# Optimization experiments

Measured on AMD Instinct MI355X. Metric: run time of the kernel, lower is better.

## Reference

```python
import jax, jax.numpy as jnp
import numpy as np

N_TOKENS = 4096
HIDDEN = 1024
FFN = 2048
N_EXPERTS = 8
TOP_K = 2


def setup_inputs() -> dict:
    key = jax.random.key(0)
    k1, k2, k3, k4 = jax.random.split(key, 4)
    x = jax.random.normal(k1, (N_TOKENS, HIDDEN), dtype=jnp.float32)
    router_weight = jax.random.normal(k2, (HIDDEN, N_EXPERTS), dtype=jnp.float32)
    # matches torch.randn(...) * 0.02 init scale
    w1 = jax.random.normal(k3, (HIDDEN, FFN * N_EXPERTS), dtype=jnp.float32) * 0.02
    w2 = jax.random.normal(k4, (FFN * N_EXPERTS, HIDDEN), dtype=jnp.float32) * 0.02
    return {"x": x, "router_weight": router_weight, "w1": w1, "w2": w2, "top_k": TOP_K}


def reference(x, router_weight, w1, w2, top_k):
    # x: [N, H]; router_weight: [H, E]; w1: [H, E*F]; w2: [E*F, H]
    N, H = x.shape
    E = router_weight.shape[1]
    F = w1.shape[1] // E

    # --- routing (router in fp32, softmax over experts, top-k probs) ---
    logits = x.astype(jnp.float32) @ router_weight            # [N, E]
    probs = jax.nn.softmax(logits, axis=-1)                   # [N, E]
    topk_probs, topk_idx = jax.lax.top_k(probs, top_k)        # [N, k]

    # --- expert FFN: per-expert gelu(x @ w1_e) @ w2_e ---
    # Dense formulation: compute every expert for every token, then gather the
    # top-k outputs per token. Same math as grouped-GEMM dispatch/combine.
    h = jax.nn.gelu(x @ w1, approximate=False)                # [N, E*F]
    h = h.reshape(N, E, F)
    w2e = w2.reshape(E, F, H)
    y = jnp.einsum('nef,efh->neh', h, w2e)                    # [N, E, H]

    # --- combine: weight selected expert outputs by router probs, sum top-k ---
    sel = jnp.take_along_axis(y, topk_idx[:, :, None], axis=1)   # [N, k, H]
    out = (sel * topk_probs[:, :, None].astype(sel.dtype)).sum(axis=1)  # [N, H]
    return out
```

## Files before the change

### kernel.cpp

```cpp
#include <hip/hip_runtime.h>
#include <hip/hip_bf16.h>
#include <math.h>

#define N_TOK 4096
#define HID   1024
#define FFN   2048
#define NEXP  8
#define WROW  (NEXP*FFN)
#define NSLOT (N_TOK*2)
#define NCHUNK (NSLOT/64)

typedef __attribute__((ext_vector_type(4))) float f32x4;
typedef __attribute__((ext_vector_type(8))) short short8;

__device__ inline unsigned short f2bf(float f) {
  union { float f; unsigned u; } v; v.f = f;
  unsigned r = v.u + 0x7fffu + ((v.u >> 16) & 1u);
  return (unsigned short)(r >> 16);
}
__device__ __forceinline__ float bf2f(unsigned short u) {
  union { unsigned u; float f; } v; v.u = ((unsigned)u) << 16; return v.f;
}

__device__ __forceinline__ void gload16(const void* g, void* l) {
  __builtin_amdgcn_global_load_lds((const __attribute__((address_space(1))) void*)g,
                                   (__attribute__((address_space(3))) void*)l, 16, 0, 0);
}

__global__ __launch_bounds__(256) void router_kernel(
    const float* __restrict__ x, const float* __restrict__ rw,
    int* __restrict__ eidx, float* __restrict__ probs,
    unsigned short* __restrict__ xb) {
  __shared__ float rwT[NEXP][HID];
  const int t = threadIdx.x;
  #pragma unroll
  for (int it = 0; it < 8; ++it) {
    const int flat = t * 4 + it * 1024;
    const f32x4 v = *(const f32x4*)&rw[flat];
    #pragma unroll
    for (int j = 0; j < 4; ++j) rwT[(flat + j) & 7][(flat + j) >> 3] = v[j];
  }
  __syncthreads();

  const int w = t >> 6, l = t & 63;
  const int n = blockIdx.x * 4 + w;
  const float* xr = x + (size_t)n * HID;
  float acc[NEXP];
  #pragma unroll
  for (int e = 0; e < NEXP; ++e) acc[e] = 0.f;

  #pragma unroll
  for (int j = 0; j < 4; ++j) {
    const int i = l * 4 + j * 256;
    const f32x4 xv = *(const f32x4*)&xr[i];
    if (xb) {
      ushort4 o;
      o.x = f2bf(xv[0]); o.y = f2bf(xv[1]); o.z = f2bf(xv[2]); o.w = f2bf(xv[3]);
      *(ushort4*)&xb[(size_t)n * HID + i] = o;
    }
    #pragma unroll
    for (int e = 0; e < NEXP; ++e) {
      const f32x4 wv = *(const f32x4*)&rwT[e][i];
      acc[e] += xv[0] * wv[0] + xv[1] * wv[1] + xv[2] * wv[2] + xv[3] * wv[3];
    }
  }
  #pragma unroll
  for (int e = 0; e < NEXP; ++e) {
    float s = acc[e];
    #pragma unroll
    for (int off = 32; off; off >>= 1) s += __shfl_xor(s, off);
    acc[e] = s;
  }
  if (l == 0) {
    float m = acc[0];
    #pragma unroll
    for (int e = 1; e < NEXP; ++e) m = fmaxf(m, acc[e]);
    float p[NEXP]; float den = 0.f;
    #pragma unroll
    for (int e = 0; e < NEXP; ++e) { p[e] = expf(acc[e] - m); den += p[e]; }
    const float inv = 1.f / den;
    int e1 = 0; float b1 = -1.f;
    #pragma unroll
    for (int e = 0; e < NEXP; ++e) if (p[e] > b1) { b1 = p[e]; e1 = e; }
    int e2 = 0; float b2 = -1.f;
    #pragma unroll
    for (int e = 0; e < NEXP; ++e) if (e != e1 && p[e] > b2) { b2 = p[e]; e2 = e; }
    eidx[n * 2 + 0] = e1; eidx[n * 2 + 1] = e2;
    probs[n * 2 + 0] = b1 * inv; probs[n * 2 + 1] = b2 * inv;
  }
}

__global__ __launch_bounds__(256) void dispatch_kernel(
    const int* __restrict__ eidx, const float* __restrict__ probs,
    int* __restrict__ counts, int* __restrict__ offs,
    int* __restrict__ rowtok, float* __restrict__ rowprob,
    int* __restrict__ tokslot) {
  __shared__ int chunkbase[NCHUNK][NEXP];
  __shared__ int tot[NEXP], off_s[NEXP];
  const int t = threadIdx.x;
  const int w = t >> 6, l = t & 63;

  for (int c = w; c < NCHUNK; c += 4) {
    const int e = eidx[c * 64 + l];
    #pragma unroll
    for (int xp = 0; xp < NEXP; ++xp) {
      const unsigned long long m = __ballot(e == xp);
      if (l == xp) chunkbase[c][xp] = __popcll(m);
    }
  }
  __syncthreads();

  if (t < NEXP) {
    int a = 0;
    for (int c = 0; c < NCHUNK; ++c) {
      const int v = chunkbase[c][t];
      chunkbase[c][t] = a;
      a += v;
    }
    tot[t] = a;
  }
  __syncthreads();
  if (t == 0) {
    int a = 0;
    for (int e = 0; e < NEXP; ++e) { off_s[e] = a; offs[e] = a; counts[e] = tot[e]; a += tot[e]; }
  }
  __syncthreads();

  for (int c = w; c < NCHUNK; c += 4) {
    const int s = c * 64 + l;
    const int e = eidx[s];
    unsigned long long mask_e = 0;
    #pragma unroll
    for (int xp = 0; xp < NEXP; ++xp) {
      const unsigned long long m = __ballot(e == xp);
      if (e == xp) mask_e = m;
    }
    const unsigned long long below = mask_e & ((1ull << l) - 1ull);
    const int pos = off_s[e] + chunkbase[c][e] + __popcll(below);
    rowtok[pos]  = s >> 1;
    rowprob[pos] = probs[s];
    tokslot[s]   = pos;
  }
}

__global__ __launch_bounds__(256) void tconv_kernel(
    const float* __restrict__ in, unsigned short* __restrict__ out,
    int R, int C, int RB) {
  __shared__ float tile[64][65];
  const int r0 = blockIdx.y * 64, c0 = blockIdx.x * 64;
  const int t = threadIdx.x;
  const int tr = t >> 4;
  const int tc4 = (t & 15) * 4;
  #pragma unroll
  for (int i = 0; i < 4; ++i) {
    const int r = tr + i * 16;
    const f32x4 v = *(const f32x4*)&in[(size_t)(r0 + r) * C + c0 + tc4];
    tile[r][tc4 + 0] = v[0]; tile[r][tc4 + 1] = v[1];
    tile[r][tc4 + 2] = v[2]; tile[r][tc4 + 3] = v[3];
  }
  __syncthreads();
  const int eb  = r0 / RB;
  const int rm0 = r0 % RB;
  #pragma unroll
  for (int i = 0; i < 4; ++i) {
    const int c = tr + i * 16;
    ushort4 o;
    o.x = f2bf(tile[tc4 + 0][c]); o.y = f2bf(tile[tc4 + 1][c]);
    o.z = f2bf(tile[tc4 + 2][c]); o.w = f2bf(tile[tc4 + 3][c]);
    const size_t oidx = (size_t)eb * C * RB + (size_t)(c0 + c) * RB + rm0 + tc4;
    *(ushort4*)&out[oidx] = o;
  }
}

__global__ __launch_bounds__(256) void gemm1_fast(
    const unsigned short* __restrict__ xb, const unsigned short* __restrict__ w1t,
    const int* __restrict__ rowtok, const int* __restrict__ counts,
    const int* __restrict__ offs, unsigned short* __restrict__ h1) {
  const int e   = blockIdx.z;
  const int cnt = counts[e];
  const int m0  = blockIdx.y * 128;
  if (m0 >= cnt) return;
  const int n0  = blockIdx.x * 128;
  const int seg = offs[e];

  __shared__ alignas(16) unsigned short Al[128 * 32];
  __shared__ alignas(16) unsigned short Bl[128 * 32];

  const int t  = threadIdx.x;
  const int l  = t & 63;
  const int w  = t >> 6;
  const int wr = w >> 1, wc = w & 1;
  const int lr = l & 15, hi = l >> 4;

  const int rowS = t >> 2;
  const int kc   = (t & 3) * 8;
  const int ra0 = m0 + rowS      < cnt ? m0 + rowS      : cnt - 1;
  const int ra1 = m0 + rowS + 64 < cnt ? m0 + rowS + 64 : cnt - 1;
  const unsigned short* aptr0 = xb + (size_t)rowtok[seg + ra0] * HID + kc;
  const unsigned short* aptr1 = xb + (size_t)rowtok[seg + ra1] * HID + kc;
  const unsigned short* bptr0 = w1t + ((size_t)e * FFN + n0 + rowS)      * HID + kc;
  const unsigned short* bptr1 = w1t + ((size_t)e * FFN + n0 + rowS + 64) * HID + kc;
  unsigned short* const ldsA0 = Al + (t & 192) * 8;
  unsigned short* const ldsB0 = Bl + (t & 192) * 8;

  f32x4 acc[4][4];
  #pragma unroll
  for (int i = 0; i < 4; ++i)
    #pragma unroll
    for (int j = 0; j < 4; ++j) acc[i][j] = (f32x4){0.f, 0.f, 0.f, 0.f};

  for (int k0 = 0; k0 < HID; k0 += 32) {
    gload16(aptr0 + k0, ldsA0);
    gload16(aptr1 + k0, ldsA0 + 2048);
    gload16(bptr0 + k0, ldsB0);
    gload16(bptr1 + k0, ldsB0 + 2048);
    __syncthreads();
    short8 af[4], bfr[4];
    #pragma unroll
    for (int mi = 0; mi < 4; ++mi) af[mi]  = *(const short8*)&Al[(wr * 64 + mi * 16 + lr) * 32 + hi * 8];
    #pragma unroll
    for (int ni = 0; ni < 4; ++ni) bfr[ni] = *(const short8*)&Bl[(wc * 64 + ni * 16 + lr) * 32 + hi * 8];
    #pragma unroll
    for (int mi = 0; mi < 4; ++mi)
      #pragma unroll
      for (int ni = 0; ni < 4; ++ni)
        acc[mi][ni] = __builtin_amdgcn_mfma_f32_16x16x32_bf16(af[mi], bfr[ni], acc[mi][ni], 0, 0, 0);
    __syncthreads();
  }

  #pragma unroll
  for (int mi = 0; mi < 4; ++mi) {
    #pragma unroll
    for (int r = 0; r < 4; ++r) {
      const int grow = m0 + wr * 64 + mi * 16 + hi * 4 + r;
      if (grow < cnt) {
        const size_t rowoff = (size_t)(seg + grow) * FFN + n0 + wc * 64 + lr;
        #pragma unroll
        for (int ni = 0; ni < 4; ++ni) {
          const float v = acc[mi][ni][r];
          const float g = 0.5f * v * (1.0f + erff(v * 0.70710678118654752f));
          h1[rowoff + ni * 16] = f2bf(g);
        }
      }
    }
  }
}

template<int KS>
__global__ __launch_bounds__(256) void gemm2_fast(
    const unsigned short* __restrict__ h1, const unsigned short* __restrict__ w2t,
    const int* __restrict__ counts, const int* __restrict__ offs,
    unsigned short* __restrict__ y) {
  const int e   = blockIdx.z & 7;
  const int kz  = blockIdx.z >> 3;
  const int cnt = counts[e];
  const int m0  = blockIdx.y * 128;
  if (m0 >= cnt) return;
  const int n0  = blockIdx.x * 128;
  const int seg = offs[e];
  constexpr int KLEN = FFN / KS;
  const int kbase = kz * KLEN;

  __shared__ alignas(16) unsigned short Al[128 * 32];
  __shared__ alignas(16) unsigned short Bl[128 * 32];

  const int t  = threadIdx.x;
  const int l  = t & 63;
  const int w  = t >> 6;
  const int wr = w >> 1, wc = w & 1;
  const int lr = l & 15, hi = l >> 4;

  const int rowS = t >> 2;
  const int kc   = (t & 3) * 8;
  const int ra0 = m0 + rowS      < cnt ? m0 + rowS      : cnt - 1;
  const int ra1 = m0 + rowS + 64 < cnt ? m0 + rowS + 64 : cnt - 1;
  const unsigned short* aptr0 = h1 + (size_t)(seg + ra0) * FFN + kbase + kc;
  const unsigned short* aptr1 = h1 + (size_t)(seg + ra1) * FFN + kbase + kc;
  const unsigned short* bptr0 = w2t + ((size_t)e * HID + n0 + rowS)      * FFN + kbase + kc;
  const unsigned short* bptr1 = w2t + ((size_t)e * HID + n0 + rowS + 64) * FFN + kbase + kc;
  unsigned short* const ldsA0 = Al + (t & 192) * 8;
  unsigned short* const ldsB0 = Bl + (t & 192) * 8;

  f32x4 acc[4][4];
  #pragma unroll
  for (int i = 0; i < 4; ++i)
    #pragma unroll
    for (int j = 0; j < 4; ++j) acc[i][j] = (f32x4){0.f, 0.f, 0.f, 0.f};

  for (int k0 = 0; k0 < KLEN; k0 += 32) {
    gload16(aptr0 + k0, ldsA0);
    gload16(aptr1 + k0, ldsA0 + 2048);
    gload16(bptr0 + k0, ldsB0);
    gload16(bptr1 + k0, ldsB0 + 2048);
    __syncthreads();
    short8 af[4], bfr[4];
    #pragma unroll
    for (int mi = 0; mi < 4; ++mi) af[mi]  = *(const short8*)&Al[(wr * 64 + mi * 16 + lr) * 32 + hi * 8];
    #pragma unroll
    for (int ni = 0; ni < 4; ++ni) bfr[ni] = *(const short8*)&Bl[(wc * 64 + ni * 16 + lr) * 32 + hi * 8];
    #pragma unroll
    for (int mi = 0; mi < 4; ++mi)
      #pragma unroll
      for (int ni = 0; ni < 4; ++ni)
        acc[mi][ni] = __builtin_amdgcn_mfma_f32_16x16x32_bf16(af[mi], bfr[ni], acc[mi][ni], 0, 0, 0);
    __syncthreads();
  }

  #pragma unroll
  for (int mi = 0; mi < 4; ++mi) {
    #pragma unroll
    for (int r = 0; r < 4; ++r) {
      const int grow = m0 + wr * 64 + mi * 16 + hi * 4 + r;
      if (grow < cnt) {
        const int slot = seg + grow;
        unsigned short* yrow = y + ((size_t)kz * NSLOT + slot) * HID + n0 + wc * 64 + lr;
        #pragma unroll
        for (int ni = 0; ni < 4; ++ni)
          yrow[ni * 16] = f2bf(acc[mi][ni][r]);
      }
    }
  }
}

template<int KS>
__global__ __launch_bounds__(256) void combine_kernel(
    const unsigned short* __restrict__ y, const int* __restrict__ tokslot,
    const float* __restrict__ probs, float* __restrict__ out) {
  const int n = blockIdx.x;
  const int c = threadIdx.x * 4;
  const int s1 = tokslot[n * 2 + 0], s2 = tokslot[n * 2 + 1];
  const float p1 = probs[n * 2 + 0], p2 = probs[n * 2 + 1];
  float r0 = 0.f, r1 = 0.f, r2 = 0.f, r3 = 0.f;
  #pragma unroll
  for (int kz = 0; kz < KS; ++kz) {
    const ushort4 a = *(const ushort4*)&y[((size_t)kz * NSLOT + s1) * HID + c];
    const ushort4 b = *(const ushort4*)&y[((size_t)kz * NSLOT + s2) * HID + c];
    r0 += p1 * bf2f(a.x) + p2 * bf2f(b.x);
    r1 += p1 * bf2f(a.y) + p2 * bf2f(b.y);
    r2 += p1 * bf2f(a.z) + p2 * bf2f(b.z);
    r3 += p1 * bf2f(a.w) + p2 * bf2f(b.w);
  }
  *(f32x4*)&out[(size_t)n * HID + c] = (f32x4){r0, r1, r2, r3};
}

__global__ __launch_bounds__(256) void gemm2_fast_atomic(
    const unsigned short* __restrict__ h1, const unsigned short* __restrict__ w2t,
    const int* __restrict__ rowtok, const float* __restrict__ rowprob,
    const int* __restrict__ counts, const int* __restrict__ offs,
    float* __restrict__ out) {
  const int e   = blockIdx.z;
  const int cnt = counts[e];
  const int m0  = blockIdx.y * 128;
  if (m0 >= cnt) return;
  const int n0  = blockIdx.x * 128;
  const int seg = offs[e];

  __shared__ alignas(16) unsigned short Al[128 * 32];
  __shared__ alignas(16) unsigned short Bl[128 * 32];

  const int t  = threadIdx.x;
  const int l  = t & 63;
  const int w  = t >> 6;
  const int wr = w >> 1, wc = w & 1;
  const int lr = l & 15, hi = l >> 4;

  const int rowS = t >> 2;
  const int kc   = (t & 3) * 8;
  const int ra0 = m0 + rowS      < cnt ? m0 + rowS      : cnt - 1;
  const int ra1 = m0 + rowS + 64 < cnt ? m0 + rowS + 64 : cnt - 1;
  const unsigned short* aptr0 = h1 + (size_t)(seg + ra0) * FFN + kc;
  const unsigned short* aptr1 = h1 + (size_t)(seg + ra1) * FFN + kc;
  const unsigned short* bptr0 = w2t + ((size_t)e * HID + n0 + rowS)      * FFN + kc;
  const unsigned short* bptr1 = w2t + ((size_t)e * HID + n0 + rowS + 64) * FFN + kc;
  unsigned short* const ldsA0 = Al + (t & 192) * 8;
  unsigned short* const ldsB0 = Bl + (t & 192) * 8;

  f32x4 acc[4][4];
  #pragma unroll
  for (int i = 0; i < 4; ++i)
    #pragma unroll
    for (int j = 0; j < 4; ++j) acc[i][j] = (f32x4){0.f, 0.f, 0.f, 0.f};

  for (int k0 = 0; k0 < FFN; k0 += 32) {
    gload16(aptr0 + k0, ldsA0);
    gload16(aptr1 + k0, ldsA0 + 2048);
    gload16(bptr0 + k0, ldsB0);
    gload16(bptr1 + k0, ldsB0 + 2048);
    __syncthreads();
    short8 af[4], bfr[4];
    #pragma unroll
    for (int mi = 0; mi < 4; ++mi) af[mi]  = *(const short8*)&Al[(wr * 64 + mi * 16 + lr) * 32 + hi * 8];
    #pragma unroll
    for (int ni = 0; ni < 4; ++ni) bfr[ni] = *(const short8*)&Bl[(wc * 64 + ni * 16 + lr) * 32 + hi * 8];
    #pragma unroll
    for (int mi = 0; mi < 4; ++mi)
      #pragma unroll
      for (int ni = 0; ni < 4; ++ni)
        acc[mi][ni] = __builtin_amdgcn_mfma_f32_16x16x32_bf16(af[mi], bfr[ni], acc[mi][ni], 0, 0, 0);
    __syncthreads();
  }

  #pragma unroll
  for (int mi = 0; mi < 4; ++mi) {
    #pragma unroll
    for (int r = 0; r < 4; ++r) {
      const int grow = m0 + wr * 64 + mi * 16 + hi * 4 + r;
      if (grow < cnt) {
        const int slot = seg + grow;
        const int tok  = rowtok[slot];
        const float p  = rowprob[slot];
        #pragma unroll
        for (int ni = 0; ni < 4; ++ni)
          atomicAdd(&out[(size_t)tok * HID + n0 + wc * 64 + ni * 16 + lr], p * acc[mi][ni][r]);
      }
    }
  }
}

__global__ __launch_bounds__(256) void gemm1_old(
    const float* __restrict__ x, const float* __restrict__ w1,
    const int* __restrict__ rowtok, const int* __restrict__ counts,
    const int* __restrict__ offs, unsigned short* __restrict__ h1) {
  const int e   = blockIdx.z;
  const int cnt = counts[e];
  const int m0  = blockIdx.y * 64;
  if (m0 >= cnt) return;
  const int n0  = blockIdx.x * 64;
  const int seg = offs[e];
  __shared__ unsigned short Al[64 * 40];
  __shared__ unsigned short Bl[64 * 40];
  const int t  = threadIdx.x;
  const int l  = t & 63;
  const int wv = t >> 6;
  const int wr = wv >> 1, wc = wv & 1;
  const int am  = t >> 2;
  const int akb = (t & 3) * 8;
  const int amg = m0 + am;
  const bool aval = (amg < cnt);
  const float* aptr = aval ? (x + (size_t)rowtok[seg + amg] * HID + akb) : x;
  const int bn  = t & 63;
  const int bkg = (t >> 6) * 8;
  const float* bptr = w1 + (size_t)e * FFN + n0 + bn;
  f32x4 acc[2][2];
  #pragma unroll
  for (int i = 0; i < 2; ++i)
    #pragma unroll
    for (int j = 0; j < 2; ++j) acc[i][j] = (f32x4){0.f, 0.f, 0.f, 0.f};
  const int kreg = (l >> 4) * 8;
  const int lr   = l & 15;
  for (int k0 = 0; k0 < HID; k0 += 32) {
    short8 av = (short8){0,0,0,0,0,0,0,0};
    if (aval) {
      const f32x4 v0 = *(const f32x4*)(aptr + k0);
      const f32x4 v1 = *(const f32x4*)(aptr + k0 + 4);
      #pragma unroll
      for (int j = 0; j < 4; ++j) { av[j] = (short)f2bf(v0[j]); av[4 + j] = (short)f2bf(v1[j]); }
    }
    *(short8*)&Al[am * 40 + akb] = av;
    short8 bv;
    #pragma unroll
    for (int j = 0; j < 8; ++j) bv[j] = (short)f2bf(bptr[(size_t)(k0 + bkg + j) * WROW]);
    *(short8*)&Bl[bn * 40 + bkg] = bv;
    __syncthreads();
    short8 af[2], bfr[2];
    #pragma unroll
    for (int mi = 0; mi < 2; ++mi) af[mi]  = *(const short8*)&Al[(wr * 32 + mi * 16 + lr) * 40 + kreg];
    #pragma unroll
    for (int ni = 0; ni < 2; ++ni) bfr[ni] = *(const short8*)&Bl[(wc * 32 + ni * 16 + lr) * 40 + kreg];
    #pragma unroll
    for (int mi = 0; mi < 2; ++mi)
      #pragma unroll
      for (int ni = 0; ni < 2; ++ni)
        acc[mi][ni] = __builtin_amdgcn_mfma_f32_16x16x32_bf16(af[mi], bfr[ni], acc[mi][ni], 0, 0, 0);
    __syncthreads();
  }
  const int kq = l >> 4;
  #pragma unroll
  for (int mi = 0; mi < 2; ++mi) {
    #pragma unroll
    for (int r = 0; r < 4; ++r) {
      const int grow = m0 + wr * 32 + mi * 16 + kq * 4 + r;
      if (grow < cnt) {
        #pragma unroll
        for (int ni = 0; ni < 2; ++ni) {
          const float v = acc[mi][ni][r];
          const float g = 0.5f * v * (1.0f + erff(v * 0.70710678118654752f));
          h1[(size_t)(seg + grow) * FFN + n0 + wc * 32 + ni * 16 + lr] = f2bf(g);
        }
      }
    }
  }
}

__global__ __launch_bounds__(256) void gemm2_old(
    const unsigned short* __restrict__ h1, const float* __restrict__ w2,
    const int* __restrict__ rowtok, const float* __restrict__ rowprob,
    const int* __restrict__ counts, const int* __restrict__ offs,
    float* __restrict__ out) {
  const int e   = blockIdx.z;
  const int cnt = counts[e];
  const int m0  = blockIdx.y * 64;
  if (m0 >= cnt) return;
  const int n0  = blockIdx.x * 64;
  const int seg = offs[e];
  __shared__ unsigned short Al[64 * 40];
  __shared__ unsigned short Bl[64 * 40];
  const int t  = threadIdx.x;
  const int l  = t & 63;
  const int wv = t >> 6;
  const int wr = wv >> 1, wc = wv & 1;
  const int am  = t >> 2;
  const int akb = (t & 3) * 8;
  const int amg = m0 + am;
  const bool aval = (amg < cnt);
  const unsigned short* aptr = aval ? (h1 + (size_t)(seg + amg) * FFN + akb) : h1;
  const int bn  = t & 63;
  const int bkg = (t >> 6) * 8;
  const float* bptr = w2 + (size_t)e * FFN * HID + n0 + bn;
  f32x4 acc[2][2];
  #pragma unroll
  for (int i = 0; i < 2; ++i)
    #pragma unroll
    for (int j = 0; j < 2; ++j) acc[i][j] = (f32x4){0.f, 0.f, 0.f, 0.f};
  const int kreg = (l >> 4) * 8;
  const int lr   = l & 15;
  for (int k0 = 0; k0 < FFN; k0 += 32) {
    short8 av = (short8){0,0,0,0,0,0,0,0};
    if (aval) av = *(const short8*)(aptr + k0);
    *(short8*)&Al[am * 40 + akb] = av;
    short8 bv;
    #pragma unroll
    for (int j = 0; j < 8; ++j) bv[j] = (short)f2bf(bptr[(size_t)(k0 + bkg + j) * HID]);
    *(short8*)&Bl[bn * 40 + bkg] = bv;
    __syncthreads();
    short8 af[2], bfr[2];
    #pragma unroll
    for (int mi = 0; mi < 2; ++mi) af[mi]  = *(const short8*)&Al[(wr * 32 + mi * 16 + lr) * 40 + kreg];
    #pragma unroll
    for (int ni = 0; ni < 2; ++ni) bfr[ni] = *(const short8*)&Bl[(wc * 32 + ni * 16 + lr) * 40 + kreg];
    #pragma unroll
    for (int mi = 0; mi < 2; ++mi)
      #pragma unroll
      for (int ni = 0; ni < 2; ++ni)
        acc[mi][ni] = __builtin_amdgcn_mfma_f32_16x16x32_bf16(af[mi], bfr[ni], acc[mi][ni], 0, 0, 0);
    __syncthreads();
  }
  const int kq = l >> 4;
  #pragma unroll
  for (int mi = 0; mi < 2; ++mi) {
    #pragma unroll
    for (int r = 0; r < 4; ++r) {
      const int grow = m0 + wr * 32 + mi * 16 + kq * 4 + r;
      if (grow < cnt) {
        const int slot = seg + grow;
        const int tok  = rowtok[slot];
        const float p  = rowprob[slot];
        #pragma unroll
        for (int ni = 0; ni < 2; ++ni)
          atomicAdd(&out[(size_t)tok * HID + n0 + wc * 32 + ni * 16 + lr], p * acc[mi][ni][r]);
      }
    }
  }
}

extern "C" void kernel_launch(void* const* d_in, const int* in_sizes, int n_in,
                              void* d_out, int out_size, void* d_ws, size_t ws_size,
                              hipStream_t stream) {
  const float* x  = (const float*)d_in[0];
  const float* rw = (const float*)d_in[1];
  const float* w1 = (const float*)d_in[2];
  const float* w2 = (const float*)d_in[3];
  float* out = (float*)d_out;

  int*   counts  = (int*)d_ws;
  int*   offs    = counts + 8;
  int*   tokslot = counts + 16;
  int*   eidx    = tokslot + NSLOT;
  float* probs   = (float*)(eidx + NSLOT);
  int*   rowtok  = (int*)(probs + NSLOT);
  float* rowprob = (float*)(rowtok + NSLOT);
  unsigned short* h1 = (unsigned short*)(rowprob + NSLOT);
  unsigned short* xb = h1 + (size_t)NSLOT * FFN;
  unsigned short* wt = xb + (size_t)N_TOK * HID;
  unsigned short* y  = wt + (size_t)WROW * HID;

  const size_t need_base = (size_t)((char*)y - (char*)d_ws);
  const size_t need_y1   = need_base + (size_t)NSLOT * HID * 2;
  const size_t need_y2   = need_base + (size_t)2 * NSLOT * HID * 2;
  const bool fast = (ws_size >= need_base);

  router_kernel<<<N_TOK / 4, 256, 0, stream>>>(x, rw, eidx, probs, fast ? xb : nullptr);
  dispatch_kernel<<<1, 256, 0, stream>>>(eidx, probs, counts, offs, rowtok, rowprob, tokslot);

  if (fast) {
    tconv_kernel<<<dim3(WROW / 64, HID / 64), 256, 0, stream>>>(w1, wt, HID, WROW, HID);
    gemm1_fast<<<dim3(FFN / 128, NSLOT / 128, NEXP), 256, 0, stream>>>(xb, wt, rowtok, counts, offs, h1);
    tconv_kernel<<<dim3(HID / 64, WROW / 64), 256, 0, stream>>>(w2, wt, WROW, HID, FFN);
    if (ws_size >= need_y2) {
      gemm2_fast<2><<<dim3(HID / 128, NSLOT / 128, NEXP * 2), 256, 0, stream>>>(h1, wt, counts, offs, y);
      combine_kernel<2><<<N_TOK, 256, 0, stream>>>(y, tokslot, probs, out);
    } else if (ws_size >= need_y1) {
      gemm2_fast<1><<<dim3(HID / 128, NSLOT / 128, NEXP), 256, 0, stream>>>(h1, wt, counts, offs, y);
      combine_kernel<1><<<N_TOK, 256, 0, stream>>>(y, tokslot, probs, out);
    } else {
      hipMemsetAsync(d_out, 0, (size_t)out_size * sizeof(float), stream);
      gemm2_fast_atomic<<<dim3(HID / 128, NSLOT / 128, NEXP), 256, 0, stream>>>(h1, wt, rowtok, rowprob, counts, offs, out);
    }
  } else {
    hipMemsetAsync(d_out, 0, (size_t)out_size * sizeof(float), stream);
    gemm1_old<<<dim3(FFN / 64, NSLOT / 64, NEXP), 256, 0, stream>>>(x, w1, rowtok, counts, offs, h1);
    gemm2_old<<<dim3(HID / 64, NSLOT / 64, NEXP), 256, 0, stream>>>(h1, w2, rowtok, rowprob, counts, offs, out);
  }
}
```

Measured before the change: 223.1 us.

## Double-buffer LDS tiles in expert GEMMs and use fast tanh-form GELU

```diff
diff --git a/kernel.cpp b/kernel.cpp
--- a/kernel.cpp
+++ b/kernel.cpp
@@ -20,6 +20,11 @@
 }
 __device__ __forceinline__ float bf2f(unsigned short u) {
   union { unsigned u; float f; } v; v.u = ((unsigned)u) << 16; return v.f;
+}
+
+__device__ __forceinline__ float gelu_f(float v) {
+  const float u = 1.5957691216057308f * v + 0.07135481627f * (v * v * v);
+  return v / (1.f + __expf(-u));
 }
 
 __device__ __forceinline__ void gload16(const void* g, void* l) {
@@ -183,8 +188,8 @@
   const int n0  = blockIdx.x * 128;
   const int seg = offs[e];
 
-  __shared__ alignas(16) unsigned short Al[128 * 32];
-  __shared__ alignas(16) unsigned short Bl[128 * 32];
+  __shared__ alignas(16) unsigned short Al[2][128 * 32];
+  __shared__ alignas(16) unsigned short Bl[2][128 * 32];
 
   const int t  = threadIdx.x;
   const int l  = t & 63;
@@ -200,8 +205,7 @@
   const unsigned short* aptr1 = xb + (size_t)rowtok[seg + ra1] * HID + kc;
   const unsigned short* bptr0 = w1t + ((size_t)e * FFN + n0 + rowS)      * HID + kc;
   const unsigned short* bptr1 = w1t + ((size_t)e * FFN + n0 + rowS + 64) * HID + kc;
-  unsigned short* const ldsA0 = Al + (t & 192) * 8;
-  unsigned short* const ldsB0 = Bl + (t & 192) * 8;
+  const int ldst = (t & 192) * 8;
 
   f32x4 acc[4][4];
   #pragma unroll
@@ -209,22 +213,33 @@
     #pragma unroll
     for (int j = 0; j < 4; ++j) acc[i][j] = (f32x4){0.f, 0.f, 0.f, 0.f};
 
-  for (int k0 = 0; k0 < HID; k0 += 32) {
-    gload16(aptr0 + k0, ldsA0);
-    gload16(aptr1 + k0, ldsA0 + 2048);
-    gload16(bptr0 + k0, ldsB0);
-    gload16(bptr1 + k0, ldsB0 + 2048);
-    __syncthreads();
+  auto STAGE = [&](int b, int k0) {
+    gload16(aptr0 + k0, &Al[b][ldst]);
+    gload16(aptr1 + k0, &Al[b][ldst + 2048]);
+    gload16(bptr0 + k0, &Bl[b][ldst]);
+    gload16(bptr1 + k0, &Bl[b][ldst + 2048]);
+  };
+  auto COMPUTE = [&](int b) {
     short8 af[4], bfr[4];
     #pragma unroll
-    for (int mi = 0; mi < 4; ++mi) af[mi]  = *(const short8*)&Al[(wr * 64 + mi * 16 + lr) * 32 + hi * 8];
-    #pragma unroll
-    for (int ni = 0; ni < 4; ++ni) bfr[ni] = *(const short8*)&Bl[(wc * 64 + ni * 16 + lr) * 32 + hi * 8];
+    for (int mi = 0; mi < 4; ++mi) af[mi]  = *(const short8*)&Al[b][(wr * 64 + mi * 16 + lr) * 32 + hi * 8];
+    #pragma unroll
+    for (int ni = 0; ni < 4; ++ni) bfr[ni] = *(const short8*)&Bl[b][(wc * 64 + ni * 16 + lr) * 32 + hi * 8];
     #pragma unroll
     for (int mi = 0; mi < 4; ++mi)
       #pragma unroll
       for (int ni = 0; ni < 4; ++ni)
         acc[mi][ni] = __builtin_amdgcn_mfma_f32_16x16x32_bf16(af[mi], bfr[ni], acc[mi][ni], 0, 0, 0);
+  };
+
+  STAGE(0, 0);
+  __syncthreads();
+  for (int k0 = 0; k0 < HID; k0 += 64) {
+    STAGE(1, k0 + 32);
+    COMPUTE(0);
+    __syncthreads();
+    if (k0 + 64 < HID) STAGE(0, k0 + 64);
+    COMPUTE(1);
     __syncthreads();
   }
 
@@ -236,11 +251,8 @@
       if (grow < cnt) {
         const size_t rowoff = (size_t)(seg + grow) * FFN + n0 + wc * 64 + lr;
         #pragma unroll
-        for (int ni = 0; ni < 4; ++ni) {
-          const float v = acc[mi][ni][r];
-          const float g = 0.5f * v * (1.0f + erff(v * 0.70710678118654752f));
-          h1[rowoff + ni * 16] = f2bf(g);
-        }
+        for (int ni = 0; ni < 4; ++ni)
+          h1[rowoff + ni * 16] = f2bf(gelu_f(acc[mi][ni][r]));
       }
     }
   }
@@ -261,8 +273,8 @@
   constexpr int KLEN = FFN / KS;
   const int kbase = kz * KLEN;
 
-  __shared__ alignas(16) unsigned short Al[128 * 32];
-  __shared__ alignas(16) unsigned short Bl[128 * 32];
+  __shared__ alignas(16) unsigned short Al[2][128 * 32];
+  __shared__ alignas(16) unsigned short Bl[2][128 * 32];
 
   const int t  = threadIdx.x;
   const int l  = t & 63;
@@ -278,8 +290,7 @@
   const unsigned short* aptr1 = h1 + (size_t)(seg + ra1) * FFN + kbase + kc;
   const unsigned short* bptr0 = w2t + ((size_t)e * HID + n0 + rowS)      * FFN + kbase + kc;
   const unsigned short* bptr1 = w2t + ((size_t)e * HID + n0 + rowS + 64) * FFN + kbase + kc;
-  unsigned short* const ldsA0 = Al + (t & 192) * 8;
-  unsigned short* const ldsB0 = Bl + (t & 192) * 8;
+  const int ldst = (t & 192) * 8;
 
   f32x4 acc[4][4];
   #pragma unroll
@@ -287,22 +298,33 @@
     #pragma unroll
     for (int j = 0; j < 4; ++j) acc[i][j] = (f32x4){0.f, 0.f, 0.f, 0.f};
 
-  for (int k0 = 0; k0 < KLEN; k0 += 32) {
-    gload16(aptr0 + k0, ldsA0);
-    gload16(aptr1 + k0, ldsA0 + 2048);
-    gload16(bptr0 + k0, ldsB0);
-    gload16(bptr1 + k0, ldsB0 + 2048);
-    __syncthreads();
+  auto STAGE = [&](int b, int k0) {
+    gload16(aptr0 + k0, &Al[b][ldst]);
+    gload16(aptr1 + k0, &Al[b][ldst + 2048]);
+    gload16(bptr0 + k0, &Bl[b][ldst]);
+    gload16(bptr1 + k0, &Bl[b][ldst + 2048]);
+  };
+  auto COMPUTE = [&](int b) {
     short8 af[4], bfr[4];
     #pragma unroll
-    for (int mi = 0; mi < 4; ++mi) af[mi]  = *(const short8*)&Al[(wr * 64 + mi * 16 + lr) * 32 + hi * 8];
-    #pragma unroll
-    for (int ni = 0; ni < 4; ++ni) bfr[ni] = *(const short8*)&Bl[(wc * 64 + ni * 16 + lr) * 32 + hi * 8];
+    for (int mi = 0; mi < 4; ++mi) af[mi]  = *(const short8*)&Al[b][(wr * 64 + mi * 16 + lr) * 32 + hi * 8];
+    #pragma unroll
+    for (int ni = 0; ni < 4; ++ni) bfr[ni] = *(const short8*)&Bl[b][(wc * 64 + ni * 16 + lr) * 32 + hi * 8];
     #pragma unroll
     for (int mi = 0; mi < 4; ++mi)
       #pragma unroll
       for (int ni = 0; ni < 4; ++ni)
         acc[mi][ni] = __builtin_amdgcn_mfma_f32_16x16x32_bf16(af[mi], bfr[ni], acc[mi][ni], 0, 0, 0);
+  };
+
+  STAGE(0, 0);
+  __syncthreads();
+  for (int k0 = 0; k0 < KLEN; k0 += 64) {
+    STAGE(1, k0 + 32);
+    COMPUTE(0);
+    __syncthreads();
+    if (k0 + 64 < KLEN) STAGE(0, k0 + 64);
+    COMPUTE(1);
     __syncthreads();
   }
 
```

Measured after the change: 219.3 us. Within noise of the previous version (-1.7%).
